# Performance work log

Measured on AMD Instinct MI355X. Metric: run time of the kernel, lower is better.

Reference implementation:

```python
import jax, jax.numpy as jnp
import numpy as np

GROUP = 16  # quantization group size along in_features
EPS = 1e-5


def setup_inputs() -> dict:
    key = jax.random.key(0)
    ks = jax.random.split(key, 6)
    B, D, L, R = 16384, 1024, 18, 32
    x = jax.random.normal(ks[0], (B, D), dtype=jnp.float32)
    # 4-bit codes in [0,16); shifted by -8 at dequant time -> values in [-8,7]
    wq = jax.random.randint(ks[1], (L, D, D), 0, 16, dtype=jnp.int32)
    # per-group positive scales, small so dequantized weights are O(0.1)
    scales = jax.random.uniform(ks[2], (L, D, D // GROUP), dtype=jnp.float32) * 0.05 + 0.005
    bias = jax.random.normal(ks[3], (L, D), dtype=jnp.float32) * 0.02
    # LoRA weights are zero-init in the module; use small random values so the
    # low-rank path is numerically exercised
    lora_a = jax.random.normal(ks[4], (L, R, D), dtype=jnp.float32) * 0.02
    lora_b = jax.random.normal(ks[5], (L, D, R), dtype=jnp.float32) * 0.02
    ln_gamma = jnp.ones((5, D), dtype=jnp.float32)
    ln_beta = jnp.zeros((5, D), dtype=jnp.float32)
    return {"x": x, "wq": wq, "scales": scales, "bias": bias,
            "lora_a": lora_a, "lora_b": lora_b,
            "ln_gamma": ln_gamma, "ln_beta": ln_beta}


def _dequant(wq_i, sc_i):
    # wq_i: [out, in] int codes; sc_i: [out, in//GROUP]
    O, I = wq_i.shape
    q = wq_i.astype(jnp.float32) - 8.0
    w = q.reshape(O, I // GROUP, GROUP) * sc_i[:, :, None]
    return w.reshape(O, I)


def _qlora(x, wq_i, sc_i, b_i, a_i, bm_i):
    w = _dequant(wq_i, sc_i)                       # [out, in]
    base = x @ w.T + b_i                           # frozen 4-bit base path
    lora = (x @ a_i.T) @ bm_i.T                    # low-rank adapter path
    return base + lora


def _layernorm(x, g, b):
    m = jnp.mean(x, axis=-1, keepdims=True)
    v = jnp.mean(jnp.square(x - m), axis=-1, keepdims=True)
    return (x - m) * jax.lax.rsqrt(v + EPS) * g + b


def reference(x, wq, scales, bias, lora_a, lora_b, ln_gamma, ln_beta):
    h = x
    for j in range(6):  # 6 residual blocks, 3 QLoRA layers each
        i = 3 * j
        r = h
        h = jax.nn.relu(_qlora(h, wq[i], scales[i], bias[i], lora_a[i], lora_b[i]))
        h = jax.nn.relu(_qlora(h, wq[i + 1], scales[i + 1], bias[i + 1], lora_a[i + 1], lora_b[i + 1]))
        h = _qlora(h, wq[i + 2], scales[i + 2], bias[i + 2], lora_a[i + 2], lora_b[i + 2])
        h = h + r
        if j < 5:
            h = _layernorm(h, ln_gamma[j], ln_beta[j])
    return h
```

## Files before the change

kernel.cpp:

```cpp
#include <hip/hip_runtime.h>
#include <hip/hip_bf16.h>
#include <stdint.h>

using bf16 = __hip_bfloat16;
typedef __attribute__((ext_vector_type(8))) short bf16x8;
typedef __attribute__((ext_vector_type(8))) unsigned short u16x8;
typedef __attribute__((ext_vector_type(4))) float f32x4;

#define B_ROWS 16384
#define D_DIM  1024
#define NLAYER 18

__device__ inline void gload_lds16(const bf16* g, bf16* l) {
    __builtin_amdgcn_global_load_lds(
        (const __attribute__((address_space(1))) void*)g,
        (__attribute__((address_space(3))) void*)l, 16, 0, 0);
}

__device__ inline unsigned short f2bf_bits(float f) {
    bf16 h = __float2bfloat16(f);
    return *reinterpret_cast<unsigned short*>(&h);
}
__device__ inline float bfbits2f(unsigned short u) {
    unsigned int x = ((unsigned int)u) << 16;
    return __uint_as_float(x);
}
__device__ inline void split_bf(float v, unsigned short& hi, unsigned short& lo) {
    hi = f2bf_bits(v);
    float hf = bfbits2f(hi);
    lo = f2bf_bits(v - hf);
}

__global__ __launch_bounds__(256)
void build_weff(const int* __restrict__ wq, const float* __restrict__ scales,
                const float* __restrict__ lora_a, const float* __restrict__ lora_b,
                bf16* __restrict__ weff_h, bf16* __restrict__ weff_l)
{
    const int lo_ = blockIdx.x;
    const int l = lo_ >> 10;
    const int o = lo_ & 1023;
    __shared__ float bsh[32];
    if (threadIdx.x < 32)
        bsh[threadIdx.x] = lora_b[((size_t)l * 1024 + o) * 32 + threadIdx.x];
    __syncthreads();

    const int*   wqrow = wq + ((size_t)l * 1024 + o) * 1024;
    const float* srow  = scales + ((size_t)l * 1024 + o) * 64;
    const float* abase = lora_a + (size_t)l * 32 * 1024;
    bf16* wh = weff_h + ((size_t)l * 1024 + o) * 1024;
    bf16* wl = weff_l + ((size_t)l * 1024 + o) * 1024;

    const int i0 = threadIdx.x * 4;
    float acc0 = 0.f, acc1 = 0.f, acc2 = 0.f, acc3 = 0.f;
    #pragma unroll
    for (int r = 0; r < 32; ++r) {
        float br = bsh[r];
        float4 av = *reinterpret_cast<const float4*>(abase + (size_t)r * 1024 + i0);
        acc0 += br * av.x; acc1 += br * av.y; acc2 += br * av.z; acc3 += br * av.w;
    }
    int4 q = *reinterpret_cast<const int4*>(wqrow + i0);
    float sc = srow[i0 >> 4];
    float w0 = (q.x - 8) * sc + acc0;
    float w1 = (q.y - 8) * sc + acc1;
    float w2 = (q.z - 8) * sc + acc2;
    float w3 = (q.w - 8) * sc + acc3;
    ushort4 uh, ul;
    split_bf(w0, uh.x, ul.x); split_bf(w1, uh.y, ul.y);
    split_bf(w2, uh.z, ul.z); split_bf(w3, uh.w, ul.w);
    *reinterpret_cast<ushort4*>(wh + i0) = uh;
    *reinterpret_cast<ushort4*>(wl + i0) = ul;
}

__global__ __launch_bounds__(256)
void cast_split(const float* __restrict__ x, bf16* __restrict__ yh, bf16* __restrict__ yl)
{
    size_t i = ((size_t)blockIdx.x * 256 + threadIdx.x) * 4;
    float4 v = *reinterpret_cast<const float4*>(x + i);
    ushort4 uh, ul;
    split_bf(v.x, uh.x, ul.x); split_bf(v.y, uh.y, ul.y);
    split_bf(v.z, uh.z, ul.z); split_bf(v.w, uh.w, ul.w);
    *reinterpret_cast<ushort4*>(yh + i) = uh;
    *reinterpret_cast<ushort4*>(yl + i) = ul;
}

#define TILE_E 4096
#define SET_E  (4 * TILE_E)

#define SCHED0 __builtin_amdgcn_sched_barrier(0)

template<int MODE>
__global__ __launch_bounds__(256)
void qgemm3(const bf16* __restrict__ AH, const bf16* __restrict__ AL,
            const bf16* __restrict__ WH, const bf16* __restrict__ WL,
            const float* __restrict__ bias,
            const bf16* __restrict__ RH, const bf16* __restrict__ RL,
            bf16* __restrict__ OH, bf16* __restrict__ OL,
            float* __restrict__ Of)
{
    __shared__ bf16 smem[2 * SET_E];

    const int b  = blockIdx.x;
    const int sb = ((b & 7) << 7) | (b >> 3);
    const int n0 = (sb & 7) * 128;
    const int m0 = (sb >> 3) * 128;

    const int tid  = threadIdx.x;
    const int wave = tid >> 6;
    const int lane = tid & 63;
    const int wr = wave >> 1, wc = wave & 1;

    const int rl = lane >> 2;
    const int ps = lane & 3;
    const int fr = lane & 15;
    const int fq = lane >> 4;

    f32x4 acc[4][4] = {};

    auto stage = [&](int buf, int k0) {
        bf16* base = smem + buf * SET_E;
        #pragma unroll
        for (int t = 0; t < 2; ++t) {
            int s = wave * 2 + t;
            int r = s * 16 + rl;
            int q = ps ^ (r & 3) ^ ((r >> 2) & 3);
            size_t ga = (size_t)(m0 + r) * D_DIM + k0 + q * 8;
            size_t gb = (size_t)(n0 + r) * D_DIM + k0 + q * 8;
            bf16* dst = base + s * 512;
            gload_lds16(AH + ga, dst);
            gload_lds16(AL + ga, dst + TILE_E);
            gload_lds16(WH + gb, dst + 2 * TILE_E);
            gload_lds16(WL + gb, dst + 3 * TILE_E);
        }
    };

    stage(0, 0);
    stage(1, 32);

    int cur = 0;
    #pragma unroll 1
    for (int kt = 0; kt < 32; ++kt) {
        SCHED0;
        if (kt <= 30) asm volatile("s_waitcnt vmcnt(8)" ::: "memory");
        else          asm volatile("s_waitcnt vmcnt(0)" ::: "memory");
        SCHED0;
        __builtin_amdgcn_s_barrier();

        const bf16* tb = smem + cur * SET_E;
        bf16x8 ah[4], al[4], bh[4], bl[4];
        #pragma unroll
        for (int m = 0; m < 4; ++m) {
            int R = wr * 64 + m * 16 + fr;
            int p = fq ^ (R & 3) ^ ((R >> 2) & 3);
            int off = R * 32 + p * 8;
            ah[m] = *reinterpret_cast<const bf16x8*>(tb + off);
            al[m] = *reinterpret_cast<const bf16x8*>(tb + TILE_E + off);
        }
        #pragma unroll
        for (int n = 0; n < 4; ++n) {
            int R = wc * 64 + n * 16 + fr;
            int p = fq ^ (R & 3) ^ ((R >> 2) & 3);
            int off = R * 32 + p * 8;
            bh[n] = *reinterpret_cast<const bf16x8*>(tb + 2 * TILE_E + off);
            bl[n] = *reinterpret_cast<const bf16x8*>(tb + 3 * TILE_E + off);
        }
        SCHED0;
        asm volatile("s_waitcnt lgkmcnt(0)" ::: "memory");
        SCHED0;
        __builtin_amdgcn_s_barrier();

        if (kt <= 29)
            stage(cur, (kt + 2) * 32);

        __builtin_amdgcn_s_setprio(1);
        #pragma unroll
        for (int m = 0; m < 4; ++m)
            #pragma unroll
            for (int n = 0; n < 4; ++n) {
                acc[m][n] = __builtin_amdgcn_mfma_f32_16x16x32_bf16(ah[m], bh[n], acc[m][n], 0, 0, 0);
                acc[m][n] = __builtin_amdgcn_mfma_f32_16x16x32_bf16(ah[m], bl[n], acc[m][n], 0, 0, 0);
                acc[m][n] = __builtin_amdgcn_mfma_f32_16x16x32_bf16(al[m], bh[n], acc[m][n], 0, 0, 0);
            }
        __builtin_amdgcn_s_setprio(0);
        cur ^= 1;
    }

    const int crow4 = (lane >> 4) * 4;
    float* cwave = reinterpret_cast<float*>(smem) + wave * 4096;

    #pragma unroll
    for (int n = 0; n < 4; ++n) {
        const float bv = bias[n0 + wc * 64 + n * 16 + fr];
        const int lcol = n * 16 + fr;
        const int chunk = lcol >> 2;
        #pragma unroll
        for (int m = 0; m < 4; ++m) {
            #pragma unroll
            for (int j = 0; j < 4; ++j) {
                const int lrow = m * 16 + crow4 + j;
                float v = acc[m][n][j] + bv;
                if (MODE == 0) v = v > 0.f ? v : 0.f;
                cwave[lrow * 64 + (chunk ^ (lrow & 15)) * 4 + (lcol & 3)] = v;
            }
        }
    }
    SCHED0;
    asm volatile("s_waitcnt lgkmcnt(0)" ::: "memory");
    SCHED0;

    const int rloc = lane >> 3;
    const int cloc = (lane & 7) * 8;
    #pragma unroll
    for (int pass = 0; pass < 8; ++pass) {
        const int lrow = pass * 8 + rloc;
        const int grow = m0 + wr * 64 + lrow;
        const size_t gbase = (size_t)grow * D_DIM + (n0 + wc * 64 + cloc);
        const int c0 = cloc >> 2;
        float4 v0 = *reinterpret_cast<const float4*>(&cwave[lrow * 64 + ((c0    ) ^ (lrow & 15)) * 4]);
        float4 v1 = *reinterpret_cast<const float4*>(&cwave[lrow * 64 + ((c0 + 1) ^ (lrow & 15)) * 4]);
        float vv[8] = {v0.x, v0.y, v0.z, v0.w, v1.x, v1.y, v1.z, v1.w};
        if (MODE != 0) {
            u16x8 rh = *reinterpret_cast<const u16x8*>(&RH[gbase]);
            u16x8 rl2 = *reinterpret_cast<const u16x8*>(&RL[gbase]);
            #pragma unroll
            for (int k = 0; k < 8; ++k)
                vv[k] += bfbits2f(rh[k]) + bfbits2f(rl2[k]);
        }
        if (MODE == 2) {
            *reinterpret_cast<float4*>(&Of[gbase])     = make_float4(vv[0], vv[1], vv[2], vv[3]);
            *reinterpret_cast<float4*>(&Of[gbase + 4]) = make_float4(vv[4], vv[5], vv[6], vv[7]);
        } else {
            u16x8 ho, lo2;
            #pragma unroll
            for (int k = 0; k < 8; ++k) {
                unsigned short h, l2;
                split_bf(vv[k], h, l2);
                ho[k] = h; lo2[k] = l2;
            }
            *reinterpret_cast<u16x8*>(&OH[gbase]) = ho;
            *reinterpret_cast<u16x8*>(&OL[gbase]) = lo2;
        }
    }
}

__global__ __launch_bounds__(256)
void ln_pair(const bf16* __restrict__ XH, const bf16* __restrict__ XL,
             bf16* __restrict__ YH, bf16* __restrict__ YL,
             const float* __restrict__ gamma, const float* __restrict__ beta)
{
    const int row = blockIdx.x;
    const int tid = threadIdx.x;
    const int lane = tid & 63;
    const int wave = tid >> 6;

    ushort4 uh = reinterpret_cast<const ushort4*>(XH + (size_t)row * D_DIM)[tid];
    ushort4 ul = reinterpret_cast<const ushort4*>(XL + (size_t)row * D_DIM)[tid];
    float v0 = bfbits2f(uh.x) + bfbits2f(ul.x);
    float v1 = bfbits2f(uh.y) + bfbits2f(ul.y);
    float v2 = bfbits2f(uh.z) + bfbits2f(ul.z);
    float v3 = bfbits2f(uh.w) + bfbits2f(ul.w);
    float s  = v0 + v1 + v2 + v3;
    float ss = v0 * v0 + v1 * v1 + v2 * v2 + v3 * v3;
    #pragma unroll
    for (int off = 32; off >= 1; off >>= 1) {
        s  += __shfl_xor(s, off, 64);
        ss += __shfl_xor(ss, off, 64);
    }
    __shared__ float red[8];
    if (lane == 0) { red[wave] = s; red[4 + wave] = ss; }
    __syncthreads();
    float S  = red[0] + red[1] + red[2] + red[3];
    float SS = red[4] + red[5] + red[6] + red[7];
    const float mean = S * (1.0f / D_DIM);
    const float var  = SS * (1.0f / D_DIM) - mean * mean;
    const float inv  = rsqrtf(var + 1e-5f);

    const int c0 = tid * 4;
    float y0 = (v0 - mean) * inv * gamma[c0 + 0] + beta[c0 + 0];
    float y1 = (v1 - mean) * inv * gamma[c0 + 1] + beta[c0 + 1];
    float y2 = (v2 - mean) * inv * gamma[c0 + 2] + beta[c0 + 2];
    float y3 = (v3 - mean) * inv * gamma[c0 + 3] + beta[c0 + 3];
    ushort4 oh, ol;
    split_bf(y0, oh.x, ol.x); split_bf(y1, oh.y, ol.y);
    split_bf(y2, oh.z, ol.z); split_bf(y3, oh.w, ol.w);
    reinterpret_cast<ushort4*>(YH + (size_t)row * D_DIM)[tid] = oh;
    reinterpret_cast<ushort4*>(YL + (size_t)row * D_DIM)[tid] = ol;
}

extern "C" void kernel_launch(void* const* d_in, const int* in_sizes, int n_in,
                              void* d_out, int out_size, void* d_ws, size_t ws_size,
                              hipStream_t stream)
{
    const float* x      = (const float*)d_in[0];
    const int*   wq     = (const int*)d_in[1];
    const float* scales = (const float*)d_in[2];
    const float* bias   = (const float*)d_in[3];
    const float* lora_a = (const float*)d_in[4];
    const float* lora_b = (const float*)d_in[5];
    const float* ln_g   = (const float*)d_in[6];
    const float* ln_b   = (const float*)d_in[7];
    float* out = (float*)d_out;

    char* ws = (char*)d_ws;
    const size_t W_ELEMS = (size_t)NLAYER * D_DIM * D_DIM;
    const size_t H_ELEMS = (size_t)B_ROWS * D_DIM;
    bf16* WHp = (bf16*)ws;
    bf16* WLp = WHp + W_ELEMS;
    bf16* HAh = WLp + W_ELEMS;
    bf16* HAl = HAh + H_ELEMS;
    bf16* HBh = HAl + H_ELEMS;
    bf16* HBl = HBh + H_ELEMS;
    bf16* HCh = (bf16*)d_out;
    bf16* HCl = HCh + H_ELEMS;

    build_weff<<<dim3(NLAYER * 1024), dim3(256), 0, stream>>>(wq, scales, lora_a, lora_b, WHp, WLp);
    cast_split<<<dim3((B_ROWS * D_DIM) / (256 * 4)), dim3(256), 0, stream>>>(x, HAh, HAl);

    dim3 ggrid(1024);
    for (int j = 0; j < 6; ++j) {
        const int l0 = 3 * j;
        const bf16* WH0 = WHp + (size_t)l0 * D_DIM * D_DIM;
        const bf16* WL0 = WLp + (size_t)l0 * D_DIM * D_DIM;
        const bf16* WH1 = WHp + (size_t)(l0 + 1) * D_DIM * D_DIM;
        const bf16* WL1 = WLp + (size_t)(l0 + 1) * D_DIM * D_DIM;
        const bf16* WH2 = WHp + (size_t)(l0 + 2) * D_DIM * D_DIM;
        const bf16* WL2 = WLp + (size_t)(l0 + 2) * D_DIM * D_DIM;
        const float* b0 = bias + (size_t)l0 * D_DIM;
        const float* b1 = bias + (size_t)(l0 + 1) * D_DIM;
        const float* b2 = bias + (size_t)(l0 + 2) * D_DIM;
        if (j < 5) {
            qgemm3<0><<<ggrid, 256, 0, stream>>>(HAh, HAl, WH0, WL0, b0, nullptr, nullptr, HBh, HBl, nullptr);
            qgemm3<0><<<ggrid, 256, 0, stream>>>(HBh, HBl, WH1, WL1, b1, nullptr, nullptr, HCh, HCl, nullptr);
            qgemm3<1><<<ggrid, 256, 0, stream>>>(HCh, HCl, WH2, WL2, b2, HAh, HAl, HBh, HBl, nullptr);
            ln_pair<<<dim3(B_ROWS), dim3(256), 0, stream>>>(HBh, HBl, HAh, HAl,
                                                            ln_g + (size_t)j * D_DIM, ln_b + (size_t)j * D_DIM);
        } else {
            qgemm3<0><<<ggrid, 256, 0, stream>>>(HAh, HAl, WH0, WL0, b0, nullptr, nullptr, HCh, HCl, nullptr);
            qgemm3<0><<<ggrid, 256, 0, stream>>>(HCh, HCl, WH1, WL1, b1, nullptr, nullptr, HBh, HBl, nullptr);
            qgemm3<2><<<ggrid, 256, 0, stream>>>(HBh, HBl, WH2, WL2, b2, HAh, HAl, nullptr, nullptr, out);
        }
    }
}
```

Before: 2.067 ms.

## Load activation fragments directly to registers and batch weight-build rows per block

The GEMM now stages only the weight tiles (hi/lo) through LDS. Activation fragments are loaded straight from global memory into registers and double-buffered across an unrolled pair of k-steps, which removes LDS traffic and bank pressure for the A operand. Separately, build_weff processes 8 output rows per block, so each lora_a load is reused across 8 rows and the launch uses fewer blocks. The risks are uncoalesced 16-byte global loads for A, higher register pressure from two A buffers, and wait counts that must match exactly.

```diff
diff --git a/kernel.cpp b/kernel.cpp
--- a/kernel.cpp
+++ b/kernel.cpp
@@ -36,39 +36,44 @@
                 const float* __restrict__ lora_a, const float* __restrict__ lora_b,
                 bf16* __restrict__ weff_h, bf16* __restrict__ weff_l)
 {
-    const int lo_ = blockIdx.x;
-    const int l = lo_ >> 10;
-    const int o = lo_ & 1023;
-    __shared__ float bsh[32];
-    if (threadIdx.x < 32)
-        bsh[threadIdx.x] = lora_b[((size_t)l * 1024 + o) * 32 + threadIdx.x];
+    const int bb = blockIdx.x;
+    const int l  = bb >> 7;
+    const int o0 = (bb & 127) * 8;
+    __shared__ float bsh[8][32];
+    {
+        const int oo = threadIdx.x >> 5, rr = threadIdx.x & 31;
+        bsh[oo][rr] = lora_b[((size_t)l * 1024 + o0 + oo) * 32 + rr];
+    }
     __syncthreads();
 
-    const int*   wqrow = wq + ((size_t)l * 1024 + o) * 1024;
-    const float* srow  = scales + ((size_t)l * 1024 + o) * 64;
     const float* abase = lora_a + (size_t)l * 32 * 1024;
-    bf16* wh = weff_h + ((size_t)l * 1024 + o) * 1024;
-    bf16* wl = weff_l + ((size_t)l * 1024 + o) * 1024;
-
     const int i0 = threadIdx.x * 4;
-    float acc0 = 0.f, acc1 = 0.f, acc2 = 0.f, acc3 = 0.f;
+    float acc[8][4] = {};
+    #pragma unroll 4
+    for (int r = 0; r < 32; ++r) {
+        float4 av = *reinterpret_cast<const float4*>(abase + (size_t)r * 1024 + i0);
+        #pragma unroll
+        for (int o = 0; o < 8; ++o) {
+            const float br = bsh[o][r];
+            acc[o][0] += br * av.x; acc[o][1] += br * av.y;
+            acc[o][2] += br * av.z; acc[o][3] += br * av.w;
+        }
+    }
     #pragma unroll
-    for (int r = 0; r < 32; ++r) {
-        float br = bsh[r];
-        float4 av = *reinterpret_cast<const float4*>(abase + (size_t)r * 1024 + i0);
-        acc0 += br * av.x; acc1 += br * av.y; acc2 += br * av.z; acc3 += br * av.w;
-    }
-    int4 q = *reinterpret_cast<const int4*>(wqrow + i0);
-    float sc = srow[i0 >> 4];
-    float w0 = (q.x - 8) * sc + acc0;
-    float w1 = (q.y - 8) * sc + acc1;
-    float w2 = (q.z - 8) * sc + acc2;
-    float w3 = (q.w - 8) * sc + acc3;
-    ushort4 uh, ul;
-    split_bf(w0, uh.x, ul.x); split_bf(w1, uh.y, ul.y);
-    split_bf(w2, uh.z, ul.z); split_bf(w3, uh.w, ul.w);
-    *reinterpret_cast<ushort4*>(wh + i0) = uh;
-    *reinterpret_cast<ushort4*>(wl + i0) = ul;
+    for (int o = 0; o < 8; ++o) {
+        const size_t row = (size_t)l * 1024 + o0 + o;
+        int4 q = *reinterpret_cast<const int4*>(wq + row * 1024 + i0);
+        const float sc = scales[row * 64 + (i0 >> 4)];
+        float w0 = (q.x - 8) * sc + acc[o][0];
+        float w1 = (q.y - 8) * sc + acc[o][1];
+        float w2 = (q.z - 8) * sc + acc[o][2];
+        float w3 = (q.w - 8) * sc + acc[o][3];
+        ushort4 uh, ul;
+        split_bf(w0, uh.x, ul.x); split_bf(w1, uh.y, ul.y);
+        split_bf(w2, uh.z, ul.z); split_bf(w3, uh.w, ul.w);
+        *reinterpret_cast<ushort4*>(weff_h + row * 1024 + i0) = uh;
+        *reinterpret_cast<ushort4*>(weff_l + row * 1024 + i0) = ul;
+    }
 }
 
 __global__ __launch_bounds__(256)
@@ -82,9 +87,6 @@
     *reinterpret_cast<ushort4*>(yh + i) = uh;
     *reinterpret_cast<ushort4*>(yl + i) = ul;
 }
-
-#define TILE_E 4096
-#define SET_E  (4 * TILE_E)
 
 #define SCHED0 __builtin_amdgcn_sched_barrier(0)
 
@@ -97,7 +99,8 @@
             bf16* __restrict__ OH, bf16* __restrict__ OL,
             float* __restrict__ Of)
 {
-    __shared__ bf16 smem[2 * SET_E];
+    __shared__ __align__(16) char smem_raw[65536];
+    bf16* smem = reinterpret_cast<bf16*>(smem_raw);
 
     const int b  = blockIdx.x;
     const int sb = ((b & 7) << 7) | (b >> 3);
@@ -116,76 +119,87 @@
 
     f32x4 acc[4][4] = {};
 
-    auto stage = [&](int buf, int k0) {
-        bf16* base = smem + buf * SET_E;
+    auto wstage = [&](int buf, int k0) {
+        bf16* base = smem + buf * 8192;
         #pragma unroll
         for (int t = 0; t < 2; ++t) {
             int s = wave * 2 + t;
             int r = s * 16 + rl;
             int q = ps ^ (r & 3) ^ ((r >> 2) & 3);
-            size_t ga = (size_t)(m0 + r) * D_DIM + k0 + q * 8;
             size_t gb = (size_t)(n0 + r) * D_DIM + k0 + q * 8;
             bf16* dst = base + s * 512;
-            gload_lds16(AH + ga, dst);
-            gload_lds16(AL + ga, dst + TILE_E);
-            gload_lds16(WH + gb, dst + 2 * TILE_E);
-            gload_lds16(WL + gb, dst + 3 * TILE_E);
+            gload_lds16(WH + gb, dst);
+            gload_lds16(WL + gb, dst + 4096);
         }
     };
-
-    stage(0, 0);
-    stage(1, 32);
-
-    int cur = 0;
-    #pragma unroll 1
-    for (int kt = 0; kt < 32; ++kt) {
-        SCHED0;
-        if (kt <= 30) asm volatile("s_waitcnt vmcnt(8)" ::: "memory");
-        else          asm volatile("s_waitcnt vmcnt(0)" ::: "memory");
-        SCHED0;
+    auto aload = [&](bf16x8* arh, bf16x8* arl, int kcol) {
+        #pragma unroll
+        for (int m = 0; m < 4; ++m) {
+            size_t ga = (size_t)(m0 + wr * 64 + m * 16 + fr) * D_DIM + kcol + fq * 8;
+            arh[m] = *reinterpret_cast<const bf16x8*>(AH + ga);
+            arl[m] = *reinterpret_cast<const bf16x8*>(AL + ga);
+        }
+    };
+    auto kstep = [&](const bf16x8* ah, const bf16x8* al, int buf, bool dostage, int knext) {
         __builtin_amdgcn_s_barrier();
-
-        const bf16* tb = smem + cur * SET_E;
-        bf16x8 ah[4], al[4], bh[4], bl[4];
-        #pragma unroll
-        for (int m = 0; m < 4; ++m) {
-            int R = wr * 64 + m * 16 + fr;
-            int p = fq ^ (R & 3) ^ ((R >> 2) & 3);
-            int off = R * 32 + p * 8;
-            ah[m] = *reinterpret_cast<const bf16x8*>(tb + off);
-            al[m] = *reinterpret_cast<const bf16x8*>(tb + TILE_E + off);
-        }
+        const bf16* tb = smem + buf * 8192;
+        bf16x8 wfh[4], wfl[4];
         #pragma unroll
         for (int n = 0; n < 4; ++n) {
             int R = wc * 64 + n * 16 + fr;
             int p = fq ^ (R & 3) ^ ((R >> 2) & 3);
             int off = R * 32 + p * 8;
-            bh[n] = *reinterpret_cast<const bf16x8*>(tb + 2 * TILE_E + off);
-            bl[n] = *reinterpret_cast<const bf16x8*>(tb + 3 * TILE_E + off);
+            wfh[n] = *reinterpret_cast<const bf16x8*>(tb + off);
+            wfl[n] = *reinterpret_cast<const bf16x8*>(tb + 4096 + off);
         }
         SCHED0;
         asm volatile("s_waitcnt lgkmcnt(0)" ::: "memory");
         SCHED0;
         __builtin_amdgcn_s_barrier();
-
-        if (kt <= 29)
-            stage(cur, (kt + 2) * 32);
-
+        if (dostage) wstage(buf, knext);
         __builtin_amdgcn_s_setprio(1);
         #pragma unroll
         for (int m = 0; m < 4; ++m)
             #pragma unroll
             for (int n = 0; n < 4; ++n) {
-                acc[m][n] = __builtin_amdgcn_mfma_f32_16x16x32_bf16(ah[m], bh[n], acc[m][n], 0, 0, 0);
-                acc[m][n] = __builtin_amdgcn_mfma_f32_16x16x32_bf16(ah[m], bl[n], acc[m][n], 0, 0, 0);
-                acc[m][n] = __builtin_amdgcn_mfma_f32_16x16x32_bf16(al[m], bh[n], acc[m][n], 0, 0, 0);
+                acc[m][n] = __builtin_amdgcn_mfma_f32_16x16x32_bf16(ah[m], wfh[n], acc[m][n], 0, 0, 0);
+                acc[m][n] = __builtin_amdgcn_mfma_f32_16x16x32_bf16(ah[m], wfl[n], acc[m][n], 0, 0, 0);
+                acc[m][n] = __builtin_amdgcn_mfma_f32_16x16x32_bf16(al[m], wfh[n], acc[m][n], 0, 0, 0);
             }
         __builtin_amdgcn_s_setprio(0);
-        cur ^= 1;
+    };
+
+    bf16x8 a0h[4], a0l[4], a1h[4], a1l[4];
+
+    wstage(0, 0);
+    aload(a0h, a0l, 0);
+    wstage(1, 32);
+
+    #pragma unroll 1
+    for (int it = 0; it < 16; ++it) {
+        const int kt0 = 2 * it;
+        aload(a1h, a1l, (kt0 + 1) * 32);
+        SCHED0;
+        asm volatile("s_waitcnt vmcnt(12)" ::: "memory");
+        SCHED0;
+        kstep(a0h, a0l, 0, kt0 <= 29, (kt0 + 2) * 32);
+
+        const int kt1 = kt0 + 1;
+        if (it < 15) {
+            aload(a0h, a0l, (kt1 + 1) * 32);
+            SCHED0;
+            asm volatile("s_waitcnt vmcnt(12)" ::: "memory");
+            SCHED0;
+        } else {
+            SCHED0;
+            asm volatile("s_waitcnt vmcnt(0)" ::: "memory");
+            SCHED0;
+        }
+        kstep(a1h, a1l, 1, kt1 <= 29, (kt1 + 2) * 32);
     }
 
     const int crow4 = (lane >> 4) * 4;
-    float* cwave = reinterpret_cast<float*>(smem) + wave * 4096;
+    float* cwave = reinterpret_cast<float*>(smem_raw) + wave * 4096;
 
     #pragma unroll
     for (int n = 0; n < 4; ++n) {
@@ -312,7 +326,7 @@
     bf16* HCh = (bf16*)d_out;
     bf16* HCl = HCh + H_ELEMS;
 
-    build_weff<<<dim3(NLAYER * 1024), dim3(256), 0, stream>>>(wq, scales, lora_a, lora_b, WHp, WLp);
+    build_weff<<<dim3(NLAYER * 128), dim3(256), 0, stream>>>(wq, scales, lora_a, lora_b, WHp, WLp);
     cast_split<<<dim3((B_ROWS * D_DIM) / (256 * 4)), dim3(256), 0, stream>>>(x, HAh, HAl);
 
     dim3 ggrid(1024);
```

Measured after the change: 2.935 ms. 42.0% more time.

## Batch 8 output rows per build_weff block and overlap MFMAs with LDS reads

Applied to the files above, without the earlier changes.

build_weff now handles 8 output rows per block. Each lora_a float4 load is reused across 8 rows instead of one, which cuts the repeated LDS/L2 reads of the LoRA A matrix and reduces the grid by 8x. In the GEMM main loop, the B fragments are read first and half of the MFMAs are issued before the lgkmcnt wait and barrier. This overlaps the remaining A-fragment LDS reads with matrix math. The trade-off is higher register pressure in build_weff (32 accumulators per thread) and fewer blocks launched for that kernel.

```diff
diff --git a/kernel.cpp b/kernel.cpp
--- a/kernel.cpp
+++ b/kernel.cpp
@@ -36,39 +36,44 @@
                 const float* __restrict__ lora_a, const float* __restrict__ lora_b,
                 bf16* __restrict__ weff_h, bf16* __restrict__ weff_l)
 {
-    const int lo_ = blockIdx.x;
-    const int l = lo_ >> 10;
-    const int o = lo_ & 1023;
-    __shared__ float bsh[32];
-    if (threadIdx.x < 32)
-        bsh[threadIdx.x] = lora_b[((size_t)l * 1024 + o) * 32 + threadIdx.x];
+    const int bb = blockIdx.x;
+    const int l  = bb >> 7;
+    const int o0 = (bb & 127) * 8;
+    __shared__ float bsh[8][32];
+    {
+        const int oo = threadIdx.x >> 5, rr = threadIdx.x & 31;
+        bsh[oo][rr] = lora_b[((size_t)l * 1024 + o0 + oo) * 32 + rr];
+    }
     __syncthreads();
 
-    const int*   wqrow = wq + ((size_t)l * 1024 + o) * 1024;
-    const float* srow  = scales + ((size_t)l * 1024 + o) * 64;
     const float* abase = lora_a + (size_t)l * 32 * 1024;
-    bf16* wh = weff_h + ((size_t)l * 1024 + o) * 1024;
-    bf16* wl = weff_l + ((size_t)l * 1024 + o) * 1024;
-
     const int i0 = threadIdx.x * 4;
-    float acc0 = 0.f, acc1 = 0.f, acc2 = 0.f, acc3 = 0.f;
+    float acc[8][4] = {};
+    #pragma unroll 4
+    for (int r = 0; r < 32; ++r) {
+        float4 av = *reinterpret_cast<const float4*>(abase + (size_t)r * 1024 + i0);
+        #pragma unroll
+        for (int o = 0; o < 8; ++o) {
+            const float br = bsh[o][r];
+            acc[o][0] += br * av.x; acc[o][1] += br * av.y;
+            acc[o][2] += br * av.z; acc[o][3] += br * av.w;
+        }
+    }
     #pragma unroll
-    for (int r = 0; r < 32; ++r) {
-        float br = bsh[r];
-        float4 av = *reinterpret_cast<const float4*>(abase + (size_t)r * 1024 + i0);
-        acc0 += br * av.x; acc1 += br * av.y; acc2 += br * av.z; acc3 += br * av.w;
-    }
-    int4 q = *reinterpret_cast<const int4*>(wqrow + i0);
-    float sc = srow[i0 >> 4];
-    float w0 = (q.x - 8) * sc + acc0;
-    float w1 = (q.y - 8) * sc + acc1;
-    float w2 = (q.z - 8) * sc + acc2;
-    float w3 = (q.w - 8) * sc + acc3;
-    ushort4 uh, ul;
-    split_bf(w0, uh.x, ul.x); split_bf(w1, uh.y, ul.y);
-    split_bf(w2, uh.z, ul.z); split_bf(w3, uh.w, ul.w);
-    *reinterpret_cast<ushort4*>(wh + i0) = uh;
-    *reinterpret_cast<ushort4*>(wl + i0) = ul;
+    for (int o = 0; o < 8; ++o) {
+        const size_t row = (size_t)l * 1024 + o0 + o;
+        int4 q = *reinterpret_cast<const int4*>(wq + row * 1024 + i0);
+        const float sc = scales[row * 64 + (i0 >> 4)];
+        float w0 = (q.x - 8) * sc + acc[o][0];
+        float w1 = (q.y - 8) * sc + acc[o][1];
+        float w2 = (q.z - 8) * sc + acc[o][2];
+        float w3 = (q.w - 8) * sc + acc[o][3];
+        ushort4 uh, ul;
+        split_bf(w0, uh.x, ul.x); split_bf(w1, uh.y, ul.y);
+        split_bf(w2, uh.z, ul.z); split_bf(w3, uh.w, ul.w);
+        *reinterpret_cast<ushort4*>(weff_h + row * 1024 + i0) = uh;
+        *reinterpret_cast<ushort4*>(weff_l + row * 1024 + i0) = ul;
+    }
 }
 
 __global__ __launch_bounds__(256)
@@ -148,6 +153,14 @@
         const bf16* tb = smem + cur * SET_E;
         bf16x8 ah[4], al[4], bh[4], bl[4];
         #pragma unroll
+        for (int n = 0; n < 4; ++n) {
+            int R = wc * 64 + n * 16 + fr;
+            int p = fq ^ (R & 3) ^ ((R >> 2) & 3);
+            int off = R * 32 + p * 8;
+            bh[n] = *reinterpret_cast<const bf16x8*>(tb + 2 * TILE_E + off);
+            bl[n] = *reinterpret_cast<const bf16x8*>(tb + 3 * TILE_E + off);
+        }
+        #pragma unroll
         for (int m = 0; m < 4; ++m) {
             int R = wr * 64 + m * 16 + fr;
             int p = fq ^ (R & 3) ^ ((R >> 2) & 3);
@@ -155,14 +168,18 @@
             ah[m] = *reinterpret_cast<const bf16x8*>(tb + off);
             al[m] = *reinterpret_cast<const bf16x8*>(tb + TILE_E + off);
         }
-        #pragma unroll
-        for (int n = 0; n < 4; ++n) {
-            int R = wc * 64 + n * 16 + fr;
-            int p = fq ^ (R & 3) ^ ((R >> 2) & 3);
-            int off = R * 32 + p * 8;
-            bh[n] = *reinterpret_cast<const bf16x8*>(tb + 2 * TILE_E + off);
-            bl[n] = *reinterpret_cast<const bf16x8*>(tb + 3 * TILE_E + off);
-        }
+
+        __builtin_amdgcn_s_setprio(1);
+        #pragma unroll
+        for (int m = 0; m < 2; ++m)
+            #pragma unroll
+            for (int n = 0; n < 4; ++n) {
+                acc[m][n] = __builtin_amdgcn_mfma_f32_16x16x32_bf16(ah[m], bh[n], acc[m][n], 0, 0, 0);
+                acc[m][n] = __builtin_amdgcn_mfma_f32_16x16x32_bf16(ah[m], bl[n], acc[m][n], 0, 0, 0);
+                acc[m][n] = __builtin_amdgcn_mfma_f32_16x16x32_bf16(al[m], bh[n], acc[m][n], 0, 0, 0);
+            }
+        __builtin_amdgcn_s_setprio(0);
+
         SCHED0;
         asm volatile("s_waitcnt lgkmcnt(0)" ::: "memory");
         SCHED0;
@@ -173,7 +190,7 @@
 
         __builtin_amdgcn_s_setprio(1);
         #pragma unroll
-        for (int m = 0; m < 4; ++m)
+        for (int m = 2; m < 4; ++m)
             #pragma unroll
             for (int n = 0; n < 4; ++n) {
                 acc[m][n] = __builtin_amdgcn_mfma_f32_16x16x32_bf16(ah[m], bh[n], acc[m][n], 0, 0, 0);
@@ -312,7 +329,7 @@
     bf16* HCh = (bf16*)d_out;
     bf16* HCl = HCh + H_ELEMS;
 
-    build_weff<<<dim3(NLAYER * 1024), dim3(256), 0, stream>>>(wq, scales, lora_a, lora_b, WHp, WLp);
+    build_weff<<<dim3(NLAYER * 128), dim3(256), 0, stream>>>(wq, scales, lora_a, lora_b, WHp, WLp);
     cast_split<<<dim3((B_ROWS * D_DIM) / (256 * 4)), dim3(256), 0, stream>>>(x, HAh, HAl);
 
     dim3 ggrid(1024);
```

After: 1.960 ms. 5.2% less time.
